# Kernel tuning notes

Measured on AMD Instinct MI355X. Metric: run time of the kernel, lower is better.

## Reference

```python
import jax, jax.numpy as jnp
import numpy as np

B, S, D, H = 2, 2048, 768, 12
Dh = D // H  # attention_head_size = 64
NEG = -1e9


def setup_inputs() -> dict:
    key = jax.random.key(0)
    ks = jax.random.split(key, 10)
    scale = 1.0 / np.sqrt(D).astype(np.float32)
    inp = {
        "hidden_states": jax.random.normal(ks[0], (B, S, D), jnp.float32),
        "Wq": jax.random.normal(ks[1], (D, D), jnp.float32) * scale,
        "bq": jnp.zeros((D,), jnp.float32),
        "Wk": jax.random.normal(ks[2], (D, D), jnp.float32) * scale,
        "bk": jnp.zeros((D,), jnp.float32),
        "Wv": jax.random.normal(ks[3], (D, D), jnp.float32) * scale,
        "bv": jnp.zeros((D,), jnp.float32),
        "Wo": jax.random.normal(ks[4], (D, D), jnp.float32) * scale,
        "bo": jnp.zeros((D,), jnp.float32),
        "mask": jax.random.randint(ks[5], (B, S), 0, 2).astype(bool),
    }
    return inp


def _heads(x):
    # [B,S,D] -> [B,H,S,Dh]
    return x.reshape(B, S, H, Dh).transpose(0, 2, 1, 3)


def reference(hidden_states, Wq, bq, Wk, bk, Wv, bv, Wo, bo, mask):
    q = _heads(hidden_states @ Wq + bq)
    k = _heads(hidden_states @ Wk + bk)
    v = _heads(hidden_states @ Wv + bv)

    # [B,H,S,S] raw scores
    scores = jnp.einsum("bhqd,bhkd->bhqk", q, k) / np.sqrt(Dh).astype(np.float32)

    # pairwise fg mask: [B,1,S,S]; True where both query and key tokens are fg
    am = mask[:, None, :, None] & mask[:, None, None, :]

    # fg softmax: bg pairs masked to -1e9; bg softmax: fg pairs masked to -1e9
    fg_probs = jax.nn.softmax(jnp.where(am, scores, NEG), axis=-1)
    bg_probs = jnp.where(am, NEG, scores)
    bg_probs = jax.nn.softmax(bg_probs, axis=-1)

    # stitch: take fg probs at fg pairs, bg probs elsewhere (replaces boolean scatter)
    probs = jnp.where(am, fg_probs, bg_probs)

    ctx = jnp.einsum("bhqk,bhkd->bhqd", probs, v)
    ctx = ctx.transpose(0, 2, 1, 3).reshape(B, S, D)
    return ctx @ Wo + bo
```

## Files before the change

kernel.cpp:

```cpp
#include <hip/hip_runtime.h>

typedef float f32x4 __attribute__((ext_vector_type(4)));
typedef short bf16x8 __attribute__((ext_vector_type(8)));

#define MFMA16(a, b, c) __builtin_amdgcn_mfma_f32_16x16x32_bf16((a), (b), (c), 0, 0, 0)
#define WAITV4() asm volatile("s_waitcnt vmcnt(4)" ::: "memory")
#define WAITV8() asm volatile("s_waitcnt vmcnt(8)" ::: "memory")
#define WAITV0() asm volatile("s_waitcnt vmcnt(0)" ::: "memory")
#define WAITL0() asm volatile("s_waitcnt lgkmcnt(0)" ::: "memory")
#define BARRIER() __builtin_amdgcn_s_barrier()
#define SCHED0() __builtin_amdgcn_sched_barrier(0)

constexpr int S_ = 2048;
constexpr int D_ = 768;
constexpr int H_ = 12;
constexpr int DH = 64;
constexpr int B_ = 2;
constexpr int M_ = B_ * S_;
constexpr int BH = B_ * H_;

typedef unsigned short u16;
typedef unsigned int u32;

__device__ __forceinline__ u16 f2bf(float f) {
  u32 u = __builtin_bit_cast(u32, f);
  u += 0x7fffu + ((u >> 16) & 1u);
  return (u16)(u >> 16);
}
__device__ __forceinline__ u32 pack2(float a, float b) {
  return (u32)f2bf(a) | ((u32)f2bf(b) << 16);
}
__device__ __forceinline__ u32 pack2r(float lo, float hi) {
  u32 a = __builtin_bit_cast(u32, lo) + 0x8000u;
  u32 b = __builtin_bit_cast(u32, hi) + 0x8000u;
  return __builtin_amdgcn_perm(b, a, 0x07060302u);
}

__device__ __forceinline__ void gload16(const void* g, void* l) {
  __builtin_amdgcn_global_load_lds((const __attribute__((address_space(1))) u32*)g,
                                   (__attribute__((address_space(3))) u32*)l, 16, 0, 0);
}

__global__ __launch_bounds__(256) void conv_bf16(const float* __restrict__ in,
                                                 u16* __restrict__ out) {
  int i = blockIdx.x * 256 + threadIdx.x;
  float4 v = ((const float4*)in)[i];
  uint2 r;
  r.x = pack2(v.x, v.y);
  r.y = pack2(v.z, v.w);
  ((uint2*)out)[i] = r;
}

__global__ __launch_bounds__(256) void conv_wT4(const float* __restrict__ Wq,
                                                const float* __restrict__ Wk,
                                                const float* __restrict__ Wv,
                                                const float* __restrict__ Wo,
                                                u16* __restrict__ wqkv,
                                                u16* __restrict__ wo) {
  __shared__ float t[32][33];
  int z = blockIdx.z;
  const float* w = z == 0 ? Wq : z == 1 ? Wk : z == 2 ? Wv : Wo;
  u16* wt = z == 3 ? wo : wqkv + (size_t)z * D_ * D_;
  int k0 = blockIdx.x << 5, n0 = blockIdx.y << 5;
  int x = threadIdx.x & 31, y = threadIdx.x >> 5;
#pragma unroll
  for (int j = 0; j < 4; ++j) t[y + 8 * j][x] = w[(size_t)(k0 + y + 8 * j) * D_ + n0 + x];
  __syncthreads();
#pragma unroll
  for (int j = 0; j < 4; ++j) wt[(size_t)(n0 + y + 8 * j) * D_ + k0 + x] = f2bf(t[x][y + 8 * j]);
}

__global__ __launch_bounds__(256) void canon_mask(const void* __restrict__ mraw,
                                                  float* __restrict__ fm,
                                                  u32* __restrict__ mw) {
  __shared__ int isBool;
  int tid = threadIdx.x;
  if (tid == 0) isBool = 0;
  __syncthreads();
  const int* mi = (const int*)mraw;
  int v = mi[tid];
  if (v != 0 && v != 1) atomicOr(&isBool, 1);
  __syncthreads();
  const unsigned char* mb = (const unsigned char*)mraw;
  int p = blockIdx.x * 256 + tid;
  int m0, m1;
  if (isBool) { m0 = mb[2 * p]; m1 = mb[2 * p + 1]; }
  else        { m0 = mi[2 * p]; m1 = mi[2 * p + 1]; }
  fm[2 * p] = (float)m0;
  fm[2 * p + 1] = (float)m1;
  mw[p] = (m0 ? 0xFFFFu : 0u) | (m1 ? 0xFFFF0000u : 0u);
}

template <int MODE>
__global__ __launch_bounds__(256, 2) void gemm128(const u16* __restrict__ A,
                                                  const u16* __restrict__ Wt,
                                                  const float* __restrict__ bq,
                                                  const float* __restrict__ bk,
                                                  const float* __restrict__ bv,
                                                  u16* __restrict__ oq,
                                                  u16* __restrict__ ok,
                                                  u16* __restrict__ ov,
                                                  float* __restrict__ of,
                                                  float qscale) {
  constexpr int NT = D_ / 64;
  __shared__ __align__(16) u16 lA[2][128 * 64];
  __shared__ __align__(16) u16 lB[2][128 * 64];
  const int tid = threadIdx.x, w = tid >> 6, lane = tid & 63;
  const int g = lane >> 4, c = lane & 15;
  const int m0 = blockIdx.x * 128, n0 = blockIdx.y * 128;
  const int wr = w >> 1, wc = w & 1;
  const int srow = lane >> 3, scb = ((lane & 7) * 16) ^ (srow << 4);
  const int sw = (c & 7) << 4;
  const char* Ab = (const char*)A + (size_t)m0 * (D_ * 2);
  const char* Bb = (const char*)Wt + (size_t)n0 * (D_ * 2);

  auto stage = [&](int buf, int t) {
    int k0b = t * 128;
#pragma unroll
    for (int a = 0; a < 4; ++a) {
      int rr = w * 32 + a * 8;
      gload16(Ab + (size_t)(rr + srow) * (D_ * 2) + k0b + scb, &lA[buf][rr * 64]);
      gload16(Bb + (size_t)(rr + srow) * (D_ * 2) + k0b + scb, &lB[buf][rr * 64]);
    }
  };

  f32x4 acc[4][4] = {};
  auto compute = [&](int buf) {
    const char* pa = (const char*)&lA[buf][0];
    const char* pb = (const char*)&lB[buf][0];
#pragma unroll
    for (int kk = 0; kk < 2; ++kk) {
      const int cs = (kk * 64 + g * 16) ^ sw;
      bf16x8 af[4], bf[4];
#pragma unroll
      for (int i = 0; i < 4; ++i)
        af[i] = *(const bf16x8*)(pa + (wr * 64 + i * 16 + c) * 128 + cs);
#pragma unroll
      for (int j = 0; j < 4; ++j)
        bf[j] = *(const bf16x8*)(pb + (wc * 64 + j * 16 + c) * 128 + cs);
      __builtin_amdgcn_s_setprio(1);
#pragma unroll
      for (int i = 0; i < 4; ++i)
#pragma unroll
        for (int j = 0; j < 4; ++j) acc[i][j] = MFMA16(af[i], bf[j], acc[i][j]);
      __builtin_amdgcn_s_setprio(0);
    }
  };

  stage(0, 0);
  int buf = 0;
#pragma unroll 1
  for (int t = 0; t < NT; ++t) {
    if (t + 1 < NT) { stage(buf ^ 1, t + 1); WAITV8(); }
    else            { WAITV0(); }
    BARRIER(); SCHED0();
    compute(buf);
    SCHED0(); WAITL0(); BARRIER();
    buf ^= 1;
  }

  if (MODE == 0) {
    const int p = n0 / D_;
    const int nn0 = n0 - p * D_;
    const float* bias = p == 0 ? bq : p == 1 ? bk : bv;
    const float sc = p == 0 ? qscale : 1.0f;
#pragma unroll
    for (int j = 0; j < 4; ++j) {
      int nn = nn0 + wc * 64 + j * 16 + c;
      float bvv = bias[nn];
      int h = nn >> 6, d = nn & 63;
#pragma unroll
      for (int i = 0; i < 4; ++i) {
        int m = m0 + wr * 64 + i * 16 + g * 4;
        int b = m >> 11, s = m & (S_ - 1);
        if (p < 2) {
          u16* dst = (p == 0 ? oq : ok) + ((size_t)(b * H_ + h) * S_ + s) * DH + d;
#pragma unroll
          for (int r = 0; r < 4; ++r) dst[(size_t)r * DH] = f2bf((acc[i][j][r] + bvv) * sc);
        } else {
          int chunk = s >> 5, kq = (s >> 2) & 7;
          int sb = kq < 4 ? 8 * kq : 8 * (kq - 4) + 4;
          uint2 pk;
          pk.x = pack2r(acc[i][j][0] + bvv, acc[i][j][1] + bvv);
          pk.y = pack2r(acc[i][j][2] + bvv, acc[i][j][3] + bvv);
          *(uint2*)(ov + ((size_t)((b * H_ + h) * DH + d)) * S_ + chunk * 32 + sb) = pk;
        }
      }
    }
  } else {
#pragma unroll
    for (int j = 0; j < 4; ++j) {
      int n = n0 + wc * 64 + j * 16 + c;
      float bvv = bq[n];
#pragma unroll
      for (int i = 0; i < 4; ++i) {
        int m = m0 + wr * 64 + i * 16 + g * 4;
#pragma unroll
        for (int r = 0; r < 4; ++r) of[(size_t)(m + r) * D_ + n] = acc[i][j][r] + bvv;
      }
    }
  }
}

__global__ __launch_bounds__(256, 3) void attn(const u16* __restrict__ Q,
                                               const u16* __restrict__ K,
                                               const u16* __restrict__ Vt,
                                               const float* __restrict__ fm,
                                               const u32* __restrict__ mw,
                                               u16* __restrict__ ctx) {
  constexpr int NT = S_ / 64;
  __shared__ __align__(16) char smem[40960];
  char* lKb = smem;
  char* lVb = smem + 16384;
  char* lMb = smem + 32768;

  const int tid = threadIdx.x;
  const int w = tid >> 6, lane = tid & 63;
  const int g = lane >> 4, c = lane & 15;
  const int qh = w & 1, kh = w >> 1;
  const int bid = blockIdx.x;
  const int wg = (bid & 7) * 96 + (bid >> 3);
  const int qt = wg & 31, bh = wg >> 5;
  const int b = bh / H_, h = bh % H_;
  const int qbase = qt * 64 + qh * 32;

  const u16* Qp = Q + ((size_t)bh * S_ + qbase) * DH;
  const char* Kp = (const char*)(K + (size_t)bh * S_ * DH);
  const char* Vp = (const char*)(Vt + (size_t)bh * DH * S_);
  const float* fmp = fm + b * S_;
  const char* mwp = (const char*)(mw + b * (S_ / 2));

  bf16x8 qf[2][2];
#pragma unroll
  for (int qs = 0; qs < 2; ++qs)
#pragma unroll
    for (int kk = 0; kk < 2; ++kk)
      qf[qs][kk] = *(const bf16x8*)(Qp + (qs * 16 + c) * DH + kk * 32 + g * 8);

  u32 ow = (c == 0) ? 0x3F803F80u : 0u;
  uint4 owv = {ow, ow, ow, ow};
  bf16x8 onesf = __builtin_bit_cast(bf16x8, owv);

  const int srow = lane >> 3;
  const int scb = ((lane & 7) * 16) ^ (srow << 4);
  const int sw = (c & 7) << 4;
  const int r8a = w * 2, r8b = w * 2 + 1;
  const int rowA = r8a * 8 + srow, rowB = r8b * 8 + srow;

  f32x4 accf[2][4] = {}, accb[2][4] = {}, alf[2] = {}, alb[2] = {};

  auto stage = [&](int buf, int t) {
    const char* kb_ = Kp + (size_t)t * 8192;
    const char* vb_ = Vp + (size_t)t * 128;
    gload16(kb_ + (size_t)rowA * 128 + scb, lKb + buf * 8192 + r8a * 1024);
    gload16(kb_ + (size_t)rowB * 128 + scb, lKb + buf * 8192 + r8b * 1024);
    gload16(vb_ + (size_t)rowA * 4096 + scb, lVb + buf * 8192 + r8a * 1024);
    gload16(vb_ + (size_t)rowB * 4096 + scb, lVb + buf * 8192 + r8b * 1024);
  };

  auto compute = [&](int buf, int t) {
    const char* kt = lKb + buf * 8192;
    const char* vtl = lVb + buf * 8192;
    const int kc = kh;
    uint2 m01 = *(const uint2*)(lMb + t * 128 + kc * 64 + g * 8);
    uint2 m23 = *(const uint2*)(lMb + t * 128 + kc * 64 + 32 + g * 8);
    bf16x8 k00 = *(const bf16x8*)(kt + (kc * 32 + c) * 128 + ((g * 16) ^ sw));
    bf16x8 k01 = *(const bf16x8*)(kt + (kc * 32 + c) * 128 + ((64 + g * 16) ^ sw));
    bf16x8 k10 = *(const bf16x8*)(kt + (kc * 32 + 16 + c) * 128 + ((g * 16) ^ sw));
    bf16x8 k11 = *(const bf16x8*)(kt + (kc * 32 + 16 + c) * 128 + ((64 + g * 16) ^ sw));
    const int csel = (kc * 64 + g * 16) ^ sw;
    bf16x8 vf0 = *(const bf16x8*)(vtl + (0 * 16 + c) * 128 + csel);
    bf16x8 vf1 = *(const bf16x8*)(vtl + (1 * 16 + c) * 128 + csel);
    bf16x8 vf2 = *(const bf16x8*)(vtl + (2 * 16 + c) * 128 + csel);
    bf16x8 vf3 = *(const bf16x8*)(vtl + (3 * 16 + c) * 128 + csel);
#pragma unroll
    for (int qs = 0; qs < 2; ++qs) {
      f32x4 st0 = {}, st1 = {};
      __builtin_amdgcn_s_setprio(1);
      st0 = MFMA16(k00, qf[qs][0], st0);
      st0 = MFMA16(k01, qf[qs][1], st0);
      st1 = MFMA16(k10, qf[qs][0], st1);
      st1 = MFMA16(k11, qf[qs][1], st1);
      __builtin_amdgcn_s_setprio(0);
      u32 ew0 = pack2r(__builtin_amdgcn_exp2f(st0[0]), __builtin_amdgcn_exp2f(st0[1]));
      u32 ew1 = pack2r(__builtin_amdgcn_exp2f(st0[2]), __builtin_amdgcn_exp2f(st0[3]));
      u32 ew2 = pack2r(__builtin_amdgcn_exp2f(st1[0]), __builtin_amdgcn_exp2f(st1[1]));
      u32 ew3 = pack2r(__builtin_amdgcn_exp2f(st1[2]), __builtin_amdgcn_exp2f(st1[3]));
      u32 pf0 = ew0 & m01.x, pf1 = ew1 & m01.y;
      u32 pf2 = ew2 & m23.x, pf3 = ew3 & m23.y;
      uint4 pfv = {pf0, pf1, pf2, pf3};
      uint4 pbv = {ew0 ^ pf0, ew1 ^ pf1, ew2 ^ pf2, ew3 ^ pf3};
      bf16x8 paf = __builtin_bit_cast(bf16x8, pfv);
      bf16x8 pab = __builtin_bit_cast(bf16x8, pbv);
      __builtin_amdgcn_s_setprio(1);
      accf[qs][0] = MFMA16(paf, vf0, accf[qs][0]);
      accb[qs][0] = MFMA16(pab, vf0, accb[qs][0]);
      accf[qs][1] = MFMA16(paf, vf1, accf[qs][1]);
      accb[qs][1] = MFMA16(pab, vf1, accb[qs][1]);
      accf[qs][2] = MFMA16(paf, vf2, accf[qs][2]);
      accb[qs][2] = MFMA16(pab, vf2, accb[qs][2]);
      accf[qs][3] = MFMA16(paf, vf3, accf[qs][3]);
      accb[qs][3] = MFMA16(pab, vf3, accb[qs][3]);
      alf[qs] = MFMA16(paf, onesf, alf[qs]);
      alb[qs] = MFMA16(pab, onesf, alb[qs]);
      __builtin_amdgcn_s_setprio(0);
    }
  };

  gload16(mwp + w * 1024 + lane * 16, lMb + w * 1024);
  stage(0, 0);

  int buf = 0;
#pragma unroll 1
  for (int t = 0; t < NT; ++t) {
    if (t + 1 < NT) { stage(buf ^ 1, t + 1); WAITV4(); }
    else            { WAITV0(); }
    BARRIER(); SCHED0();
    compute(buf, t);
    SCHED0(); WAITL0(); BARRIER();
    buf ^= 1;
  }

  f32x4* red = (f32x4*)smem + (size_t)qh * 1280;
  if (kh == 1) {
#pragma unroll
    for (int qs = 0; qs < 2; ++qs)
#pragma unroll
      for (int n = 0; n < 4; ++n) {
        red[(qs * 4 + n) * 64 + lane] = accf[qs][n];
        red[(8 + qs * 4 + n) * 64 + lane] = accb[qs][n];
      }
    red[16 * 64 + lane] = alf[0];
    red[17 * 64 + lane] = alf[1];
    red[18 * 64 + lane] = alb[0];
    red[19 * 64 + lane] = alb[1];
  }
  __syncthreads();
  if (kh == 0) {
#pragma unroll
    for (int qs = 0; qs < 2; ++qs)
#pragma unroll
      for (int n = 0; n < 4; ++n) {
        accf[qs][n] += red[(qs * 4 + n) * 64 + lane];
        accb[qs][n] += red[(8 + qs * 4 + n) * 64 + lane];
      }
    alf[0] += red[16 * 64 + lane];
    alf[1] += red[17 * 64 + lane];
    alb[0] += red[18 * 64 + lane];
    alb[1] += red[19 * 64 + lane];

#pragma unroll
    for (int qs = 0; qs < 2; ++qs) {
      const int qw = qbase + qs * 16;
#pragma unroll
      for (int r = 0; r < 4; ++r) {
        int ql = g * 4 + r;
        float lfr = __shfl(alf[qs][r], g * 16);
        float lbr = __shfl(alb[qs][r], g * 16);
        bool fg = fmp[qw + ql] > 0.5f;
        float inv_f = (lfr > 0.f) ? 1.f / lfr : 0.f;
        float inv_b = (lbr > 0.f) ? 1.f / lbr : 0.f;
        float inv_all = 1.f / (lfr + lbr);
#pragma unroll
        for (int n = 0; n < 4; ++n) {
          float o = fg ? (accf[qs][n][r] * inv_f + accb[qs][n][r] * inv_b)
                       : ((accf[qs][n][r] + accb[qs][n][r]) * inv_all);
          ctx[((size_t)(b * S_ + qw + ql)) * D_ + h * DH + n * 16 + c] = f2bf(o);
        }
      }
    }
  }
}

extern "C" void kernel_launch(void* const* d_in, const int* in_sizes, int n_in,
                              void* d_out, int out_size, void* d_ws, size_t ws_size,
                              hipStream_t stream) {
  const float* hs = (const float*)d_in[0];
  const float* Wq = (const float*)d_in[1];
  const float* bq = (const float*)d_in[2];
  const float* Wk = (const float*)d_in[3];
  const float* bk = (const float*)d_in[4];
  const float* Wv = (const float*)d_in[5];
  const float* bv = (const float*)d_in[6];
  const float* Wo = (const float*)d_in[7];
  const float* bo = (const float*)d_in[8];
  const void* mraw = d_in[9];

  char* ws = (char*)d_ws;
  size_t off = 0;
  auto alloc = [&](size_t bytes) {
    void* p = ws + off;
    off += (bytes + 255) & ~(size_t)255;
    return p;
  };
  u16* hsb = (u16*)alloc((size_t)M_ * D_ * 2);
  u16* wqkvT = (u16*)alloc((size_t)3 * D_ * D_ * 2);
  u16* woT = (u16*)alloc((size_t)D_ * D_ * 2);
  u16* qb = (u16*)alloc((size_t)M_ * D_ * 2);
  u16* kb = (u16*)alloc((size_t)M_ * D_ * 2);
  u16* vtb = (u16*)alloc((size_t)M_ * D_ * 2);
  u16* ctx = (u16*)alloc((size_t)M_ * D_ * 2);
  float* fmf = (float*)alloc((size_t)B_ * S_ * 4);
  u32* mwb = (u32*)alloc((size_t)B_ * S_ / 2 * 4);

  conv_bf16<<<(M_ * D_ / 4 + 255) / 256, 256, 0, stream>>>(hs, hsb);
  conv_wT4<<<dim3(D_ / 32, D_ / 32, 4), 256, 0, stream>>>(Wq, Wk, Wv, Wo, wqkvT, woT);
  canon_mask<<<B_ * S_ / 512, 256, 0, stream>>>(mraw, fmf, mwb);

  const float qscale = 0.125f * 1.44269504088896f;
  gemm128<0><<<dim3(M_ / 128, 3 * D_ / 128), 256, 0, stream>>>(
      hsb, wqkvT, bq, bk, bv, qb, kb, vtb, nullptr, qscale);

  attn<<<dim3(768), 256, 0, stream>>>(qb, kb, vtb, fmf, mwb, ctx);

  gemm128<1><<<dim3(M_ / 128, D_ / 128), 256, 0, stream>>>(
      ctx, woT, bo, nullptr, nullptr, nullptr, nullptr, nullptr, (float*)d_out, 1.0f);
}
```

Before: 104.8 us.

## Split attention work across 8 waves with 16 query rows per wave

```diff
diff --git a/kernel.cpp b/kernel.cpp
--- a/kernel.cpp
+++ b/kernel.cpp
@@ -4,7 +4,7 @@
 typedef short bf16x8 __attribute__((ext_vector_type(8)));
 
 #define MFMA16(a, b, c) __builtin_amdgcn_mfma_f32_16x16x32_bf16((a), (b), (c), 0, 0, 0)
-#define WAITV4() asm volatile("s_waitcnt vmcnt(4)" ::: "memory")
+#define WAITV2() asm volatile("s_waitcnt vmcnt(2)" ::: "memory")
 #define WAITV8() asm volatile("s_waitcnt vmcnt(8)" ::: "memory")
 #define WAITV0() asm volatile("s_waitcnt vmcnt(0)" ::: "memory")
 #define WAITL0() asm volatile("s_waitcnt lgkmcnt(0)" ::: "memory")
@@ -202,7 +202,7 @@
   }
 }
 
-__global__ __launch_bounds__(256, 3) void attn(const u16* __restrict__ Q,
+__global__ __launch_bounds__(512, 4) void attn(const u16* __restrict__ Q,
                                                const u16* __restrict__ K,
                                                const u16* __restrict__ Vt,
                                                const float* __restrict__ fm,
@@ -217,25 +217,21 @@
   const int tid = threadIdx.x;
   const int w = tid >> 6, lane = tid & 63;
   const int g = lane >> 4, c = lane & 15;
-  const int qh = w & 1, kh = w >> 1;
+  const int qq = w & 3, kh = w >> 2;
   const int bid = blockIdx.x;
   const int wg = (bid & 7) * 96 + (bid >> 3);
   const int qt = wg & 31, bh = wg >> 5;
   const int b = bh / H_, h = bh % H_;
-  const int qbase = qt * 64 + qh * 32;
-
-  const u16* Qp = Q + ((size_t)bh * S_ + qbase) * DH;
+  const int qw0 = qt * 64 + qq * 16;
+
+  const u16* Qp = Q + ((size_t)bh * S_ + qw0) * DH;
   const char* Kp = (const char*)(K + (size_t)bh * S_ * DH);
   const char* Vp = (const char*)(Vt + (size_t)bh * DH * S_);
   const float* fmp = fm + b * S_;
   const char* mwp = (const char*)(mw + b * (S_ / 2));
 
-  bf16x8 qf[2][2];
-#pragma unroll
-  for (int qs = 0; qs < 2; ++qs)
-#pragma unroll
-    for (int kk = 0; kk < 2; ++kk)
-      qf[qs][kk] = *(const bf16x8*)(Qp + (qs * 16 + c) * DH + kk * 32 + g * 8);
+  bf16x8 qf0 = *(const bf16x8*)(Qp + c * DH + g * 8);
+  bf16x8 qf1 = *(const bf16x8*)(Qp + c * DH + 32 + g * 8);
 
   u32 ow = (c == 0) ? 0x3F803F80u : 0u;
   uint4 owv = {ow, ow, ow, ow};
@@ -244,18 +240,14 @@
   const int srow = lane >> 3;
   const int scb = ((lane & 7) * 16) ^ (srow << 4);
   const int sw = (c & 7) << 4;
-  const int r8a = w * 2, r8b = w * 2 + 1;
-  const int rowA = r8a * 8 + srow, rowB = r8b * 8 + srow;
-
-  f32x4 accf[2][4] = {}, accb[2][4] = {}, alf[2] = {}, alb[2] = {};
+
+  f32x4 accf[4] = {}, accb[4] = {}, alf = {}, alb = {};
 
   auto stage = [&](int buf, int t) {
     const char* kb_ = Kp + (size_t)t * 8192;
     const char* vb_ = Vp + (size_t)t * 128;
-    gload16(kb_ + (size_t)rowA * 128 + scb, lKb + buf * 8192 + r8a * 1024);
-    gload16(kb_ + (size_t)rowB * 128 + scb, lKb + buf * 8192 + r8b * 1024);
-    gload16(vb_ + (size_t)rowA * 4096 + scb, lVb + buf * 8192 + r8a * 1024);
-    gload16(vb_ + (size_t)rowB * 4096 + scb, lVb + buf * 8192 + r8b * 1024);
+    gload16(kb_ + (size_t)(w * 8 + srow) * 128 + scb, lKb + buf * 8192 + w * 1024);
+    gload16(vb_ + (size_t)(w * 8 + srow) * 4096 + scb, lVb + buf * 8192 + w * 1024);
   };
 
   auto compute = [&](int buf, int t) {
@@ -273,47 +265,44 @@
     bf16x8 vf1 = *(const bf16x8*)(vtl + (1 * 16 + c) * 128 + csel);
     bf16x8 vf2 = *(const bf16x8*)(vtl + (2 * 16 + c) * 128 + csel);
     bf16x8 vf3 = *(const bf16x8*)(vtl + (3 * 16 + c) * 128 + csel);
-#pragma unroll
-    for (int qs = 0; qs < 2; ++qs) {
-      f32x4 st0 = {}, st1 = {};
-      __builtin_amdgcn_s_setprio(1);
-      st0 = MFMA16(k00, qf[qs][0], st0);
-      st0 = MFMA16(k01, qf[qs][1], st0);
-      st1 = MFMA16(k10, qf[qs][0], st1);
-      st1 = MFMA16(k11, qf[qs][1], st1);
-      __builtin_amdgcn_s_setprio(0);
-      u32 ew0 = pack2r(__builtin_amdgcn_exp2f(st0[0]), __builtin_amdgcn_exp2f(st0[1]));
-      u32 ew1 = pack2r(__builtin_amdgcn_exp2f(st0[2]), __builtin_amdgcn_exp2f(st0[3]));
-      u32 ew2 = pack2r(__builtin_amdgcn_exp2f(st1[0]), __builtin_amdgcn_exp2f(st1[1]));
-      u32 ew3 = pack2r(__builtin_amdgcn_exp2f(st1[2]), __builtin_amdgcn_exp2f(st1[3]));
-      u32 pf0 = ew0 & m01.x, pf1 = ew1 & m01.y;
-      u32 pf2 = ew2 & m23.x, pf3 = ew3 & m23.y;
-      uint4 pfv = {pf0, pf1, pf2, pf3};
-      uint4 pbv = {ew0 ^ pf0, ew1 ^ pf1, ew2 ^ pf2, ew3 ^ pf3};
-      bf16x8 paf = __builtin_bit_cast(bf16x8, pfv);
-      bf16x8 pab = __builtin_bit_cast(bf16x8, pbv);
-      __builtin_amdgcn_s_setprio(1);
-      accf[qs][0] = MFMA16(paf, vf0, accf[qs][0]);
-      accb[qs][0] = MFMA16(pab, vf0, accb[qs][0]);
-      accf[qs][1] = MFMA16(paf, vf1, accf[qs][1]);
-      accb[qs][1] = MFMA16(pab, vf1, accb[qs][1]);
-      accf[qs][2] = MFMA16(paf, vf2, accf[qs][2]);
-      accb[qs][2] = MFMA16(pab, vf2, accb[qs][2]);
-      accf[qs][3] = MFMA16(paf, vf3, accf[qs][3]);
-      accb[qs][3] = MFMA16(pab, vf3, accb[qs][3]);
-      alf[qs] = MFMA16(paf, onesf, alf[qs]);
-      alb[qs] = MFMA16(pab, onesf, alb[qs]);
-      __builtin_amdgcn_s_setprio(0);
-    }
-  };
-
-  gload16(mwp + w * 1024 + lane * 16, lMb + w * 1024);
+    f32x4 st0 = {}, st1 = {};
+    __builtin_amdgcn_s_setprio(1);
+    st0 = MFMA16(k00, qf0, st0);
+    st0 = MFMA16(k01, qf1, st0);
+    st1 = MFMA16(k10, qf0, st1);
+    st1 = MFMA16(k11, qf1, st1);
+    __builtin_amdgcn_s_setprio(0);
+    u32 ew0 = pack2r(__builtin_amdgcn_exp2f(st0[0]), __builtin_amdgcn_exp2f(st0[1]));
+    u32 ew1 = pack2r(__builtin_amdgcn_exp2f(st0[2]), __builtin_amdgcn_exp2f(st0[3]));
+    u32 ew2 = pack2r(__builtin_amdgcn_exp2f(st1[0]), __builtin_amdgcn_exp2f(st1[1]));
+    u32 ew3 = pack2r(__builtin_amdgcn_exp2f(st1[2]), __builtin_amdgcn_exp2f(st1[3]));
+    u32 pf0 = ew0 & m01.x, pf1 = ew1 & m01.y;
+    u32 pf2 = ew2 & m23.x, pf3 = ew3 & m23.y;
+    uint4 pfv = {pf0, pf1, pf2, pf3};
+    uint4 pbv = {ew0 ^ pf0, ew1 ^ pf1, ew2 ^ pf2, ew3 ^ pf3};
+    bf16x8 paf = __builtin_bit_cast(bf16x8, pfv);
+    bf16x8 pab = __builtin_bit_cast(bf16x8, pbv);
+    __builtin_amdgcn_s_setprio(1);
+    accf[0] = MFMA16(paf, vf0, accf[0]);
+    accb[0] = MFMA16(pab, vf0, accb[0]);
+    accf[1] = MFMA16(paf, vf1, accf[1]);
+    accb[1] = MFMA16(pab, vf1, accb[1]);
+    accf[2] = MFMA16(paf, vf2, accf[2]);
+    accb[2] = MFMA16(pab, vf2, accb[2]);
+    accf[3] = MFMA16(paf, vf3, accf[3]);
+    accb[3] = MFMA16(pab, vf3, accb[3]);
+    alf = MFMA16(paf, onesf, alf);
+    alb = MFMA16(pab, onesf, alb);
+    __builtin_amdgcn_s_setprio(0);
+  };
+
+  if (w < 4) gload16(mwp + w * 1024 + lane * 16, lMb + w * 1024);
   stage(0, 0);
 
   int buf = 0;
 #pragma unroll 1
   for (int t = 0; t < NT; ++t) {
-    if (t + 1 < NT) { stage(buf ^ 1, t + 1); WAITV4(); }
+    if (t + 1 < NT) { stage(buf ^ 1, t + 1); WAITV2(); }
     else            { WAITV0(); }
     BARRIER(); SCHED0();
     compute(buf, t);
@@ -321,52 +310,40 @@
     buf ^= 1;
   }
 
-  f32x4* red = (f32x4*)smem + (size_t)qh * 1280;
+  f32x4* red = (f32x4*)(smem + (size_t)qq * 10240);
   if (kh == 1) {
 #pragma unroll
-    for (int qs = 0; qs < 2; ++qs)
-#pragma unroll
-      for (int n = 0; n < 4; ++n) {
-        red[(qs * 4 + n) * 64 + lane] = accf[qs][n];
-        red[(8 + qs * 4 + n) * 64 + lane] = accb[qs][n];
-      }
-    red[16 * 64 + lane] = alf[0];
-    red[17 * 64 + lane] = alf[1];
-    red[18 * 64 + lane] = alb[0];
-    red[19 * 64 + lane] = alb[1];
+    for (int n = 0; n < 4; ++n) {
+      red[n * 64 + lane] = accf[n];
+      red[(4 + n) * 64 + lane] = accb[n];
+    }
+    red[8 * 64 + lane] = alf;
+    red[9 * 64 + lane] = alb;
   }
   __syncthreads();
   if (kh == 0) {
 #pragma unroll
-    for (int qs = 0; qs < 2; ++qs)
+    for (int n = 0; n < 4; ++n) {
+      accf[n] += red[n * 64 + lane];
+      accb[n] += red[(4 + n) * 64 + lane];
+    }
+    alf += red[8 * 64 + lane];
+    alb += red[9 * 64 + lane];
+
+#pragma unroll
+    for (int r = 0; r < 4; ++r) {
+      int ql = g * 4 + r;
+      float lfr = __shfl(alf[r], g * 16);
+      float lbr = __shfl(alb[r], g * 16);
+      bool fg = fmp[qw0 + ql] > 0.5f;
+      float inv_f = (lfr > 0.f) ? 1.f / lfr : 0.f;
+      float inv_b = (lbr > 0.f) ? 1.f / lbr : 0.f;
+      float inv_all = 1.f / (lfr + lbr);
 #pragma unroll
       for (int n = 0; n < 4; ++n) {
-        accf[qs][n] += red[(qs * 4 + n) * 64 + lane];
-        accb[qs][n] += red[(8 + qs * 4 + n) * 64 + lane];
-      }
-    alf[0] += red[16 * 64 + lane];
-    alf[1] += red[17 * 64 + lane];
-    alb[0] += red[18 * 64 + lane];
-    alb[1] += red[19 * 64 + lane];
-
-#pragma unroll
-    for (int qs = 0; qs < 2; ++qs) {
-      const int qw = qbase + qs * 16;
-#pragma unroll
-      for (int r = 0; r < 4; ++r) {
-        int ql = g * 4 + r;
-        float lfr = __shfl(alf[qs][r], g * 16);
-        float lbr = __shfl(alb[qs][r], g * 16);
-        bool fg = fmp[qw + ql] > 0.5f;
-        float inv_f = (lfr > 0.f) ? 1.f / lfr : 0.f;
-        float inv_b = (lbr > 0.f) ? 1.f / lbr : 0.f;
-        float inv_all = 1.f / (lfr + lbr);
-#pragma unroll
-        for (int n = 0; n < 4; ++n) {
-          float o = fg ? (accf[qs][n][r] * inv_f + accb[qs][n][r] * inv_b)
-                       : ((accf[qs][n][r] + accb[qs][n][r]) * inv_all);
-          ctx[((size_t)(b * S_ + qw + ql)) * D_ + h * DH + n * 16 + c] = f2bf(o);
-        }
+        float o = fg ? (accf[n][r] * inv_f + accb[n][r] * inv_b)
+                     : ((accf[n][r] + accb[n][r]) * inv_all);
+        ctx[((size_t)(b * S_ + qw0 + ql)) * D_ + h * DH + n * 16 + c] = f2bf(o);
       }
     }
   }
@@ -411,7 +388,7 @@
   gemm128<0><<<dim3(M_ / 128, 3 * D_ / 128), 256, 0, stream>>>(
       hsb, wqkvT, bq, bk, bv, qb, kb, vtb, nullptr, qscale);
 
-  attn<<<dim3(768), 256, 0, stream>>>(qb, kb, vtb, fmf, mwb, ctx);
+  attn<<<dim3(768), 512, 0, stream>>>(qb, kb, vtb, fmf, mwb, ctx);
 
   gemm128<1><<<dim3(M_ / 128, D_ / 128), 256, 0, stream>>>(
       ctx, woT, bo, nullptr, nullptr, nullptr, nullptr, nullptr, (float*)d_out, 1.0f);
```

Measured after the change: 109.3 us. 1.04x slower.
